# Kernel optimization log

Hardware: AMD Instinct MI355X
Metric: run time of the kernel (lower is better)

Reference implementation:

```python
import jax, jax.numpy as jnp
import numpy as np

BN_EPS = 1e-5
CLAMP = 1e-4


def setup_inputs() -> dict:
    key = jax.random.key(0)
    ks = jax.random.split(key, 13)
    B, C, T, A = 32, 1536, 1000, 128
    s = 0.02  # keep conv pre-activations in a sane range
    return {
        "x": jax.random.normal(ks[0], (B, C, T), jnp.float32),
        "W1": jax.random.normal(ks[1], (A, 3 * C), jnp.float32) * s,
        "b1": jax.random.normal(ks[2], (A,), jnp.float32) * s,
        "g1": jax.random.uniform(ks[3], (A,), jnp.float32, 0.5, 1.5),
        "beta1": jax.random.normal(ks[4], (A,), jnp.float32) * 0.1,
        "rm1": jax.random.normal(ks[5], (A,), jnp.float32) * 0.1,
        "rv1": jax.random.uniform(ks[6], (A,), jnp.float32, 0.5, 1.5),
        "W2": jax.random.normal(ks[7], (C, A), jnp.float32) * s,
        "b2": jax.random.normal(ks[8], (C,), jnp.float32) * s,
        "g2": jax.random.uniform(ks[9], (C,), jnp.float32, 0.5, 1.5),
        "beta2": jax.random.normal(ks[10], (C,), jnp.float32) * 0.1,
        "rm2": jax.random.normal(ks[11], (C,), jnp.float32) * 0.1,
        "rv2": jax.random.uniform(ks[12], (C,), jnp.float32, 0.5, 1.5),
    }


def _bn(h, g, beta, rm, rv):
    # inference-mode BatchNorm1d over channel axis 1 of [B, C, T]
    inv = g / jnp.sqrt(rv + BN_EPS)
    return h * inv[None, :, None] + (beta - rm * inv)[None, :, None]


def reference(x, W1, b1, g1, beta1, rm1, rv1, W2, b2, g2, beta2, rm2, rv2):
    B, C, T = x.shape
    mean = jnp.mean(x, axis=2)                       # [B, C]
    var = jnp.var(x, axis=2, ddof=1)                 # unbiased, matches torch.var
    std = jnp.sqrt(jnp.clip(var, CLAMP, None))       # [B, C]
    # 1x1 conv over concat([x, mean.repeat(T), std.repeat(T)]) without
    # materializing the [B, 3C, T] tensor: split W1 into three channel blocks.
    Wx, Wm, Ws = W1[:, :C], W1[:, C:2 * C], W1[:, 2 * C:]
    h = jnp.einsum('oc,bct->bot', Wx, x)             # [B, A, T]
    h = h + (mean @ Wm.T + std @ Ws.T + b1)[:, :, None]
    h = jax.nn.relu(h)
    h = _bn(h, g1, beta1, rm1, rv1)
    h = jnp.tanh(h)
    h = jnp.einsum('oa,bat->bot', W2, h) + b2[None, :, None]  # [B, C, T]
    h = jax.nn.relu(h)
    h = _bn(h, g2, beta2, rm2, rv2)
    w = jax.nn.softmax(h, axis=2)                    # attention over time
    mu = jnp.sum(x * w, axis=2)                      # [B, C]
    sg = jnp.sqrt(jnp.clip(jnp.sum(x * x * w, axis=2) - mu * mu, CLAMP, None))
    return jnp.concatenate([mu, sg], axis=1)         # [B, 2C]
```

## Files before the change

kernel.cpp:

```cpp
#include <hip/hip_runtime.h>
#include <cmath>

#define BN_EPS 1e-5f
#define CLAMPV 1e-4f

static constexpr int B_ = 32, C_ = 1536, T_ = 1000, A_ = 128;
static constexpr int C3 = 3 * C_;
static constexpr int TP = 1024;
static constexpr int KS1 = C_ / 32;
static constexpr int KS2 = A_ / 32;
static constexpr int OM1 = A_ / 16;
static constexpr int OM2 = C_ / 16;

using bf16x8 = __attribute__((ext_vector_type(8))) short;
using f32x4  = __attribute__((ext_vector_type(4))) float;

#define MFMA(a, b, c) __builtin_amdgcn_mfma_f32_16x16x32_bf16(a, b, c, 0, 0, 0)

static constexpr size_t WT_OFF   = 0;
static constexpr size_t MEAN_OFF = 393216;
static constexpr size_t STD_OFF  = MEAN_OFF + 49152;
static constexpr size_t BIAS_OFF = STD_OFF + 49152;
static constexpr size_t INV1_OFF = BIAS_OFF + 4096;
static constexpr size_t SH1_OFF  = INV1_OFF + 128;
static constexpr size_t INV2_OFF = SH1_OFF + 128;
static constexpr size_t SH2_OFF  = INV2_OFF + 1536;
static constexpr size_t WXH_OFF  = SH2_OFF + 1536;
static constexpr size_t WXL_OFF  = WXH_OFF + 98304;
static constexpr size_t W2H_OFF  = WXL_OFF + 98304;
static constexpr size_t W2L_OFF  = W2H_OFF + 98304;
static constexpr size_t HTP_OFF  = W2L_OFF + 98304;
static constexpr size_t SS_OFF   = HTP_OFF + 4194304;
static constexpr size_t PP_OFF   = SS_OFF + 49152;
static constexpr size_t QQ_OFF   = PP_OFF + 49152;

__device__ __forceinline__ short f2bf(float v) {
  __bf16 b = (__bf16)v;
  return __builtin_bit_cast(short, b);
}
__device__ __forceinline__ float bf2f(short s) {
  unsigned int u = ((unsigned int)(unsigned short)s) << 16;
  return __builtin_bit_cast(float, u);
}

__global__ __launch_bounds__(256) void k_transpose(const float* __restrict__ W1,
                                                   float* __restrict__ WT) {
  __shared__ float tile[32][33];
  int c0 = blockIdx.x * 32;
  int o0 = blockIdx.y * 32;
  int tx = threadIdx.x, ty = threadIdx.y;
#pragma unroll
  for (int k = 0; k < 32; k += 8)
    tile[ty + k][tx] = W1[(size_t)(o0 + ty + k) * C3 + C_ + c0 + tx];
  __syncthreads();
#pragma unroll
  for (int k = 0; k < 32; k += 8)
    WT[(size_t)(c0 + ty + k) * A_ + o0 + tx] = tile[tx][ty + k];
}

__global__ __launch_bounds__(256) void k_stats(const float* __restrict__ x,
                                               float* __restrict__ mean,
                                               float* __restrict__ stdv) {
  int row  = blockIdx.x * 4 + (threadIdx.x >> 6);
  int lane = threadIdx.x & 63;
  const float2* xr2 = (const float2*)(x + (size_t)row * T_);
  float s1 = 0.f, s2 = 0.f;
#pragma unroll 4
  for (int j = lane; j < T_ / 2; j += 64) {
    float2 v = xr2[j];
    s1 += v.x + v.y;
    s2 += v.x * v.x + v.y * v.y;
  }
#pragma unroll
  for (int off = 32; off; off >>= 1) {
    s1 += __shfl_xor(s1, off);
    s2 += __shfl_xor(s2, off);
  }
  if (lane == 0) {
    float m   = s1 / T_;
    float var = (s2 - s1 * m) / (T_ - 1);
    mean[row] = m;
    stdv[row] = sqrtf(fmaxf(var, CLAMPV));
  }
}

__global__ void k_bn(const float* __restrict__ g1, const float* __restrict__ beta1,
                     const float* __restrict__ rm1, const float* __restrict__ rv1,
                     const float* __restrict__ g2, const float* __restrict__ beta2,
                     const float* __restrict__ rm2, const float* __restrict__ rv2,
                     float* inv1, float* sh1, float* inv2, float* sh2) {
  int i = blockIdx.x * 256 + threadIdx.x;
  if (i < A_) { float iv = g1[i] * rsqrtf(rv1[i] + BN_EPS); inv1[i] = iv; sh1[i] = beta1[i] - rm1[i] * iv; }
  if (i < C_) { float iv = g2[i] * rsqrtf(rv2[i] + BN_EPS); inv2[i] = iv; sh2[i] = beta2[i] - rm2[i] * iv; }
}

__global__ __launch_bounds__(256) void k_pack_w(const float* __restrict__ W1,
                                                const float* __restrict__ W2,
                                                unsigned short* __restrict__ WxH,
                                                unsigned short* __restrict__ WxL,
                                                unsigned short* __restrict__ W2H,
                                                unsigned short* __restrict__ W2L) {
  int id = blockIdx.x * 256 + threadIdx.x;
  if (id < OM1 * KS1 * 64) {
    int l = id & 63; int ks = (id >> 6) % KS1; int om = id / (64 * KS1);
    int o  = om * 16 + (l & 15);
    int c0 = ks * 32 + (l >> 4) * 8;
#pragma unroll
    for (int j = 0; j < 8; j++) {
      float v = W1[(size_t)o * C3 + c0 + j];
      short h = f2bf(v); float fh = bf2f(h); short lo = f2bf(v - fh);
      WxH[(size_t)id * 8 + j] = (unsigned short)h;
      WxL[(size_t)id * 8 + j] = (unsigned short)lo;
    }
  } else {
    int id2 = id - OM1 * KS1 * 64;
    int l = id2 & 63; int ks = (id2 >> 6) & 3; int om = id2 / (64 * KS2);
    int cr = om * 16 + (l & 15);
    int a0 = ks * 32 + (l >> 4) * 8;
#pragma unroll
    for (int j = 0; j < 8; j++) {
      float v = W2[(size_t)cr * A_ + a0 + j];
      short h = f2bf(v); float fh = bf2f(h); short lo = f2bf(v - fh);
      W2H[(size_t)id2 * 8 + j] = (unsigned short)h;
      W2L[(size_t)id2 * 8 + j] = (unsigned short)lo;
    }
  }
}

__global__ __launch_bounds__(128) void k_bias(const float* __restrict__ WT,
                                              const float* __restrict__ b1,
                                              const float* __restrict__ mean,
                                              const float* __restrict__ stdv,
                                              float* __restrict__ bias1) {
  __shared__ float sm[C_], ss[C_];
  int b = blockIdx.x, o = threadIdx.x;
  for (int c = o; c < C_; c += 128) { sm[c] = mean[b * C_ + c]; ss[c] = stdv[b * C_ + c]; }
  __syncthreads();
  float acc = b1[o];
#pragma unroll 8
  for (int c = 0; c < C_; c++)
    acc += sm[c] * WT[(size_t)c * A_ + o] + ss[c] * WT[(size_t)(C_ + c) * A_ + o];
  bias1[b * A_ + o] = acc;
}

__global__ __launch_bounds__(256) void k_gemm1(const float* __restrict__ x,
    const unsigned short* __restrict__ WxH, const unsigned short* __restrict__ WxL,
    const float* __restrict__ bias1, const float* __restrict__ inv1, const float* __restrict__ sh1,
    unsigned int* __restrict__ htP) {
  int b = blockIdx.x, tt = blockIdx.y;
  int wid = threadIdx.x >> 6, l = threadIdx.x & 63;
  int wm = wid >> 1, wn = wid & 1;
  int lg = l >> 4, ll = l & 15;

  f32x4 acc[4][4];
#pragma unroll
  for (int mi = 0; mi < 4; mi++)
#pragma unroll
    for (int ni = 0; ni < 4; ni++) acc[mi][ni] = (f32x4){0.f, 0.f, 0.f, 0.f};

  const float* xb = x + (size_t)b * C_ * T_;
  int tbase = tt * 128 + wn * 64;
  int   tloc[4];
  float tmask[4];
#pragma unroll
  for (int ns = 0; ns < 4; ns++) {
    int t = tbase + ns * 16 + ll;
    tloc[ns]  = t < T_ ? t : T_ - 1;
    tmask[ns] = t < T_ ? 1.f : 0.f;
  }

  for (int ks = 0; ks < KS1; ks++) {
    bf16x8 ah[4], al[4];
#pragma unroll
    for (int mi = 0; mi < 4; mi++) {
      size_t fi = ((size_t)((wm * 4 + mi) * KS1 + ks) * 64 + l) * 8;
      ah[mi] = *(const bf16x8*)(WxH + fi);
      al[mi] = *(const bf16x8*)(WxL + fi);
    }
    int cg = ks * 32 + lg * 8;
    bf16x8 bh[4], bl[4];
#pragma unroll
    for (int ns = 0; ns < 4; ns++) {
      const float* xp = xb + tloc[ns];
      float m = tmask[ns];
#pragma unroll
      for (int j = 0; j < 8; j++) {
        float v = xp[(size_t)(cg + j) * T_] * m;
        short h = f2bf(v); float fh = bf2f(h); short lo = f2bf(v - fh);
        bh[ns][j] = h; bl[ns][j] = lo;
      }
    }
#pragma unroll
    for (int mi = 0; mi < 4; mi++)
#pragma unroll
      for (int ns = 0; ns < 4; ns++) {
        acc[mi][ns] = MFMA(ah[mi], bh[ns], acc[mi][ns]);
        acc[mi][ns] = MFMA(ah[mi], bl[ns], acc[mi][ns]);
        acc[mi][ns] = MFMA(al[mi], bh[ns], acc[mi][ns]);
      }
  }

#pragma unroll
  for (int mi = 0; mi < 4; mi++) {
#pragma unroll
    for (int r = 0; r < 4; r++) {
      int o = wm * 64 + mi * 16 + lg * 4 + r;
      float bz = bias1[b * A_ + o];
      float iv = inv1[o], sv = sh1[o];
#pragma unroll
      for (int ni = 0; ni < 4; ni++) {
        int t = tbase + ni * 16 + ll;
        float v = acc[mi][ni][r] + bz;
        v = fmaxf(v, 0.f) * iv + sv;
        float e  = __expf(2.f * v);
        float th = 1.f - 2.f / (e + 1.f);
        short h = f2bf(th); float fh = bf2f(h); short lo = f2bf(th - fh);
        htP[(size_t)(b * A_ + o) * TP + t] =
            ((unsigned int)(unsigned short)h << 16) | (unsigned short)lo;
      }
    }
  }
}

__global__ __launch_bounds__(256) void k_pool(const float* __restrict__ x,
    const unsigned int* __restrict__ htP,
    const unsigned short* __restrict__ W2H, const unsigned short* __restrict__ W2L,
    const float* __restrict__ b2, const float* __restrict__ inv2, const float* __restrict__ sh2,
    float* __restrict__ SS, float* __restrict__ PP, float* __restrict__ QQ) {
  int b = blockIdx.x, cb = blockIdx.y, th = blockIdx.z;
  int wid = threadIdx.x >> 6, l = threadIdx.x & 63;
  int wm = wid >> 1, wn = wid & 1;
  int lg = l >> 4, ll = l & 15;
  int tix = threadIdx.x;

  __shared__ float sb2[128], siv[128], ssh[128];
  __shared__ float rS[2][128], rP[2][128], rQ[2][128];
  if (tix < 128) {
    int c = cb * 128 + tix;
    sb2[tix] = b2[c]; siv[tix] = inv2[c]; ssh[tix] = sh2[c];
  }
  __syncthreads();

  float S[4][4] = {}, P[4][4] = {}, Q[4][4] = {};
  const float* xb = x + (size_t)b * C_ * T_;
  const unsigned int* hb = htP + (size_t)b * A_ * TP;

  for (int tt = th * 2; tt < th * 2 + 2; tt++) {
    int tb = tt * 128 + wn * 64;
    f32x4 acc[4][4];
#pragma unroll
    for (int mi = 0; mi < 4; mi++)
#pragma unroll
      for (int ni = 0; ni < 4; ni++) acc[mi][ni] = (f32x4){0.f, 0.f, 0.f, 0.f};

    for (int ks = 0; ks < KS2; ks++) {
      bf16x8 bh[4], bl[4];
      int ag = ks * 32 + lg * 8;
#pragma unroll
      for (int ns = 0; ns < 4; ns++) {
        int t = tb + ns * 16 + ll;
#pragma unroll
        for (int j = 0; j < 8; j++) {
          unsigned int v = hb[(size_t)(ag + j) * TP + t];
          bh[ns][j] = (short)(v >> 16);
          bl[ns][j] = (short)(v & 0xffffu);
        }
      }
#pragma unroll
      for (int mi = 0; mi < 4; mi++) {
        size_t fi = ((size_t)((cb * 8 + wm * 4 + mi) * KS2 + ks) * 64 + l) * 8;
        bf16x8 ah = *(const bf16x8*)(W2H + fi);
        bf16x8 al = *(const bf16x8*)(W2L + fi);
#pragma unroll
        for (int ns = 0; ns < 4; ns++) {
          acc[mi][ns] = MFMA(ah, bh[ns], acc[mi][ns]);
          acc[mi][ns] = MFMA(ah, bl[ns], acc[mi][ns]);
          acc[mi][ns] = MFMA(al, bh[ns], acc[mi][ns]);
        }
      }
    }
#pragma unroll
    for (int ns = 0; ns < 4; ns++) {
      int t = tb + ns * 16 + ll;
      float em = t < T_ ? 1.f : 0.f;
      int   te = t < T_ ? t : T_ - 1;
#pragma unroll
      for (int mi = 0; mi < 4; mi++) {
#pragma unroll
        for (int r = 0; r < 4; r++) {
          int cl = wm * 64 + mi * 16 + lg * 4 + r;
          float h2 = acc[mi][ns][r] + sb2[cl];
          float z  = fmaxf(h2, 0.f) * siv[cl] + ssh[cl];
          float e  = __expf(z) * em;
          float xv = xb[(size_t)(cb * 128 + cl) * T_ + te];
          S[mi][r] += e; P[mi][r] += e * xv; Q[mi][r] += e * xv * xv;
        }
      }
    }
  }

#pragma unroll
  for (int mi = 0; mi < 4; mi++)
#pragma unroll
    for (int r = 0; r < 4; r++)
      for (int d = 1; d < 16; d <<= 1) {
        S[mi][r] += __shfl_xor(S[mi][r], d);
        P[mi][r] += __shfl_xor(P[mi][r], d);
        Q[mi][r] += __shfl_xor(Q[mi][r], d);
      }
  if (ll == 0) {
#pragma unroll
    for (int mi = 0; mi < 4; mi++)
#pragma unroll
      for (int r = 0; r < 4; r++) {
        int cl = wm * 64 + mi * 16 + lg * 4 + r;
        rS[wn][cl] = S[mi][r]; rP[wn][cl] = P[mi][r]; rQ[wn][cl] = Q[mi][r];
      }
  }
  __syncthreads();
  if (tix < 128) {
    int i = b * C_ + cb * 128 + tix;
    atomicAdd(&SS[i], rS[0][tix] + rS[1][tix]);
    atomicAdd(&PP[i], rP[0][tix] + rP[1][tix]);
    atomicAdd(&QQ[i], rQ[0][tix] + rQ[1][tix]);
  }
}

__global__ void k_zero(float* p, int n) {
  int i = blockIdx.x * 256 + threadIdx.x;
  if (i < n) p[i] = 0.f;
}

__global__ void k_finish(const float* __restrict__ SS, const float* __restrict__ PP,
                         const float* __restrict__ QQ, float* __restrict__ out) {
  int i = blockIdx.x * 256 + threadIdx.x;
  if (i >= B_ * C_) return;
  int b = i / C_, c = i % C_;
  float S = SS[i];
  float mu = PP[i] / S;
  float var = QQ[i] / S - mu * mu;
  out[(size_t)b * 2 * C_ + c]      = mu;
  out[(size_t)b * 2 * C_ + C_ + c] = sqrtf(fmaxf(var, CLAMPV));
}

extern "C" void kernel_launch(void* const* d_in, const int* in_sizes, int n_in,
                              void* d_out, int out_size, void* d_ws, size_t ws_size,
                              hipStream_t stream) {
  const float* x     = (const float*)d_in[0];
  const float* W1    = (const float*)d_in[1];
  const float* b1    = (const float*)d_in[2];
  const float* g1    = (const float*)d_in[3];
  const float* beta1 = (const float*)d_in[4];
  const float* rm1   = (const float*)d_in[5];
  const float* rv1   = (const float*)d_in[6];
  const float* W2    = (const float*)d_in[7];
  const float* b2    = (const float*)d_in[8];
  const float* g2    = (const float*)d_in[9];
  const float* beta2 = (const float*)d_in[10];
  const float* rm2   = (const float*)d_in[11];
  const float* rv2   = (const float*)d_in[12];

  float* ws    = (float*)d_ws;
  float* WT    = ws + WT_OFF;
  float* mean  = ws + MEAN_OFF;
  float* stdv  = ws + STD_OFF;
  float* bias1 = ws + BIAS_OFF;
  float* inv1  = ws + INV1_OFF;
  float* sh1   = ws + SH1_OFF;
  float* inv2  = ws + INV2_OFF;
  float* sh2   = ws + SH2_OFF;
  unsigned short* WxH = (unsigned short*)(ws + WXH_OFF);
  unsigned short* WxL = (unsigned short*)(ws + WXL_OFF);
  unsigned short* W2H = (unsigned short*)(ws + W2H_OFF);
  unsigned short* W2L = (unsigned short*)(ws + W2L_OFF);
  unsigned int*   htP = (unsigned int*)(ws + HTP_OFF);
  float* SS = ws + SS_OFF;
  float* PP = ws + PP_OFF;
  float* QQ = ws + QQ_OFF;
  float* out = (float*)d_out;

  k_bn<<<dim3(6), 256, 0, stream>>>(g1, beta1, rm1, rv1, g2, beta2, rm2, rv2,
                                    inv1, sh1, inv2, sh2);
  k_transpose<<<dim3(96, 4), dim3(32, 8), 0, stream>>>(W1, WT);
  k_pack_w<<<dim3(192), 256, 0, stream>>>(W1, W2, WxH, WxL, W2H, W2L);
  k_zero<<<dim3((3 * B_ * C_ + 255) / 256), 256, 0, stream>>>(SS, 3 * B_ * C_);
  k_stats<<<dim3(B_ * C_ / 4), 256, 0, stream>>>(x, mean, stdv);
  k_bias<<<dim3(B_), 128, 0, stream>>>(WT, b1, mean, stdv, bias1);
  k_gemm1<<<dim3(B_, 8), 256, 0, stream>>>(x, WxH, WxL, bias1, inv1, sh1, htP);
  k_pool<<<dim3(B_, 12, 4), 256, 0, stream>>>(x, htP, W2H, W2L, b2, inv2, sh2, SS, PP, QQ);
  k_finish<<<dim3((B_ * C_ + 255) / 256), 256, 0, stream>>>(SS, PP, QQ, out);
}
```

Baseline: 558.6 us.

## Increase parallelism across bias, GEMM1 split-K, and pool kernels

The bias reduction is split across 8 channel groups with a second reduce kernel. GEMM1 becomes a 2-way split-K with smaller time tiles, and the activation moves into a separate elementwise kernel that sums the partials. The pool kernel uses 512 threads with one time tile per block and 8 time slices, and writes per-slice partial sums instead of atomics, so the zeroing kernel is removed. The goal is more blocks to fill the GPU's compute units, at the cost of extra partial-sum memory traffic and extra launches.

```diff
diff --git a/kernel.cpp b/kernel.cpp
--- a/kernel.cpp
+++ b/kernel.cpp
@@ -17,22 +17,24 @@
 
 #define MFMA(a, b, c) __builtin_amdgcn_mfma_f32_16x16x32_bf16(a, b, c, 0, 0, 0)
 
-static constexpr size_t WT_OFF   = 0;
-static constexpr size_t MEAN_OFF = 393216;
-static constexpr size_t STD_OFF  = MEAN_OFF + 49152;
-static constexpr size_t BIAS_OFF = STD_OFF + 49152;
-static constexpr size_t INV1_OFF = BIAS_OFF + 4096;
-static constexpr size_t SH1_OFF  = INV1_OFF + 128;
-static constexpr size_t INV2_OFF = SH1_OFF + 128;
-static constexpr size_t SH2_OFF  = INV2_OFF + 1536;
-static constexpr size_t WXH_OFF  = SH2_OFF + 1536;
-static constexpr size_t WXL_OFF  = WXH_OFF + 98304;
-static constexpr size_t W2H_OFF  = WXL_OFF + 98304;
-static constexpr size_t W2L_OFF  = W2H_OFF + 98304;
-static constexpr size_t HTP_OFF  = W2L_OFF + 98304;
-static constexpr size_t SS_OFF   = HTP_OFF + 4194304;
-static constexpr size_t PP_OFF   = SS_OFF + 49152;
-static constexpr size_t QQ_OFF   = PP_OFF + 49152;
+static constexpr size_t WT_OFF    = 0;
+static constexpr size_t MEAN_OFF  = 393216;
+static constexpr size_t STD_OFF   = MEAN_OFF + 49152;
+static constexpr size_t BIASP_OFF = STD_OFF + 49152;
+static constexpr size_t BIAS_OFF  = BIASP_OFF + 32768;
+static constexpr size_t INV1_OFF  = BIAS_OFF + 4096;
+static constexpr size_t SH1_OFF   = INV1_OFF + 128;
+static constexpr size_t INV2_OFF  = SH1_OFF + 128;
+static constexpr size_t SH2_OFF   = INV2_OFF + 1536;
+static constexpr size_t WXH_OFF   = SH2_OFF + 1536;
+static constexpr size_t WXL_OFF   = WXH_OFF + 98304;
+static constexpr size_t W2H_OFF   = WXL_OFF + 98304;
+static constexpr size_t W2L_OFF   = W2H_OFF + 98304;
+static constexpr size_t HTP_OFF   = W2L_OFF + 98304;
+static constexpr size_t HPART_OFF = HTP_OFF + 4194304;
+static constexpr size_t SP_OFF    = HPART_OFF + 8388608;
+static constexpr size_t PP_OFF    = SP_OFF + 393216;
+static constexpr size_t QP_OFF    = PP_OFF + 393216;
 
 __device__ __forceinline__ short f2bf(float v) {
   __bf16 b = (__bf16)v;
@@ -127,49 +129,69 @@
   }
 }
 
-__global__ __launch_bounds__(128) void k_bias(const float* __restrict__ WT,
-                                              const float* __restrict__ b1,
-                                              const float* __restrict__ mean,
-                                              const float* __restrict__ stdv,
-                                              float* __restrict__ bias1) {
-  __shared__ float sm[C_], ss[C_];
+__global__ __launch_bounds__(256) void k_biasPart(const float* __restrict__ WT,
+                                                  const float* __restrict__ mean,
+                                                  const float* __restrict__ stdv,
+                                                  float* __restrict__ biasPart) {
+  __shared__ float sm[192], ss[192];
+  __shared__ float red[2][128];
+  int b = blockIdx.x, cg = blockIdx.y;
+  int tix = threadIdx.x;
+  if (tix < 192) {
+    sm[tix] = mean[b * C_ + cg * 192 + tix];
+    ss[tix] = stdv[b * C_ + cg * 192 + tix];
+  }
+  __syncthreads();
+  int o = tix & 127, cs = tix >> 7;
+  float acc = 0.f;
+#pragma unroll 4
+  for (int i = 0; i < 96; i++) {
+    int c = cs * 96 + i;
+    int cgl = cg * 192 + c;
+    acc += sm[c] * WT[(size_t)cgl * A_ + o] + ss[c] * WT[(size_t)(C_ + cgl) * A_ + o];
+  }
+  red[cs][o] = acc;
+  __syncthreads();
+  if (tix < 128)
+    biasPart[((size_t)cg * B_ + b) * A_ + tix] = red[0][tix] + red[1][tix];
+}
+
+__global__ void k_bias2(const float* __restrict__ b1, const float* __restrict__ biasPart,
+                        float* __restrict__ bias1) {
   int b = blockIdx.x, o = threadIdx.x;
-  for (int c = o; c < C_; c += 128) { sm[c] = mean[b * C_ + c]; ss[c] = stdv[b * C_ + c]; }
-  __syncthreads();
-  float acc = b1[o];
-#pragma unroll 8
-  for (int c = 0; c < C_; c++)
-    acc += sm[c] * WT[(size_t)c * A_ + o] + ss[c] * WT[(size_t)(C_ + c) * A_ + o];
-  bias1[b * A_ + o] = acc;
-}
-
-__global__ __launch_bounds__(256) void k_gemm1(const float* __restrict__ x,
+  float a = b1[o];
+#pragma unroll
+  for (int g = 0; g < 8; g++) a += biasPart[((size_t)g * B_ + b) * A_ + o];
+  bias1[b * A_ + o] = a;
+}
+
+__global__ __launch_bounds__(256, 4) void k_gemm1(const float* __restrict__ x,
     const unsigned short* __restrict__ WxH, const unsigned short* __restrict__ WxL,
-    const float* __restrict__ bias1, const float* __restrict__ inv1, const float* __restrict__ sh1,
-    unsigned int* __restrict__ htP) {
-  int b = blockIdx.x, tt = blockIdx.y;
+    float* __restrict__ hPart) {
+  int b = blockIdx.x, tt = blockIdx.y, kc = blockIdx.z;
   int wid = threadIdx.x >> 6, l = threadIdx.x & 63;
-  int wm = wid >> 1, wn = wid & 1;
+  int wm = wid & 1, wn = wid >> 1;
   int lg = l >> 4, ll = l & 15;
 
-  f32x4 acc[4][4];
+  f32x4 acc[4][2];
 #pragma unroll
   for (int mi = 0; mi < 4; mi++)
 #pragma unroll
-    for (int ni = 0; ni < 4; ni++) acc[mi][ni] = (f32x4){0.f, 0.f, 0.f, 0.f};
+    for (int ns = 0; ns < 2; ns++) acc[mi][ns] = (f32x4){0.f, 0.f, 0.f, 0.f};
 
   const float* xb = x + (size_t)b * C_ * T_;
-  int tbase = tt * 128 + wn * 64;
-  int   tloc[4];
-  float tmask[4];
-#pragma unroll
-  for (int ns = 0; ns < 4; ns++) {
+  int tbase = tt * 64 + wn * 32;
+  int   tloc[2];
+  float tmask[2];
+#pragma unroll
+  for (int ns = 0; ns < 2; ns++) {
     int t = tbase + ns * 16 + ll;
     tloc[ns]  = t < T_ ? t : T_ - 1;
     tmask[ns] = t < T_ ? 1.f : 0.f;
   }
 
-  for (int ks = 0; ks < KS1; ks++) {
+  for (int ksl = 0; ksl < KS1 / 2; ksl++) {
+    int ks = kc * (KS1 / 2) + ksl;
     bf16x8 ah[4], al[4];
 #pragma unroll
     for (int mi = 0; mi < 4; mi++) {
@@ -178,9 +200,9 @@
       al[mi] = *(const bf16x8*)(WxL + fi);
     }
     int cg = ks * 32 + lg * 8;
-    bf16x8 bh[4], bl[4];
-#pragma unroll
-    for (int ns = 0; ns < 4; ns++) {
+    bf16x8 bh[2], bl[2];
+#pragma unroll
+    for (int ns = 0; ns < 2; ns++) {
       const float* xp = xb + tloc[ns];
       float m = tmask[ns];
 #pragma unroll
@@ -193,7 +215,7 @@
 #pragma unroll
     for (int mi = 0; mi < 4; mi++)
 #pragma unroll
-      for (int ns = 0; ns < 4; ns++) {
+      for (int ns = 0; ns < 2; ns++) {
         acc[mi][ns] = MFMA(ah[mi], bh[ns], acc[mi][ns]);
         acc[mi][ns] = MFMA(ah[mi], bl[ns], acc[mi][ns]);
         acc[mi][ns] = MFMA(al[mi], bh[ns], acc[mi][ns]);
@@ -201,144 +223,140 @@
   }
 
 #pragma unroll
-  for (int mi = 0; mi < 4; mi++) {
+  for (int mi = 0; mi < 4; mi++)
 #pragma unroll
     for (int r = 0; r < 4; r++) {
       int o = wm * 64 + mi * 16 + lg * 4 + r;
-      float bz = bias1[b * A_ + o];
-      float iv = inv1[o], sv = sh1[o];
-#pragma unroll
-      for (int ni = 0; ni < 4; ni++) {
-        int t = tbase + ni * 16 + ll;
-        float v = acc[mi][ni][r] + bz;
-        v = fmaxf(v, 0.f) * iv + sv;
-        float e  = __expf(2.f * v);
-        float th = 1.f - 2.f / (e + 1.f);
-        short h = f2bf(th); float fh = bf2f(h); short lo = f2bf(th - fh);
-        htP[(size_t)(b * A_ + o) * TP + t] =
-            ((unsigned int)(unsigned short)h << 16) | (unsigned short)lo;
-      }
-    }
-  }
-}
-
-__global__ __launch_bounds__(256) void k_pool(const float* __restrict__ x,
+#pragma unroll
+      for (int ns = 0; ns < 2; ns++) {
+        int t = tbase + ns * 16 + ll;
+        hPart[(((size_t)kc * B_ + b) * A_ + o) * TP + t] = acc[mi][ns][r];
+      }
+    }
+}
+
+__global__ __launch_bounds__(256) void k_act(const float* __restrict__ hPart,
+                                             const float* __restrict__ bias1,
+                                             const float* __restrict__ inv1,
+                                             const float* __restrict__ sh1,
+                                             unsigned int* __restrict__ htP) {
+  int bo = blockIdx.x;
+  int t  = blockIdx.y * 256 + threadIdx.x;
+  int b = bo >> 7, o = bo & 127;
+  float v = hPart[(size_t)bo * TP + t] + hPart[((size_t)B_ * A_ + bo) * TP + t]
+          + bias1[b * A_ + o];
+  v = fmaxf(v, 0.f) * inv1[o] + sh1[o];
+  float e  = __expf(2.f * v);
+  float th = 1.f - 2.f / (e + 1.f);
+  short h = f2bf(th); float fh = bf2f(h); short lo = f2bf(th - fh);
+  htP[(size_t)bo * TP + t] = ((unsigned int)(unsigned short)h << 16) | (unsigned short)lo;
+}
+
+__global__ __launch_bounds__(512, 4) void k_pool(const float* __restrict__ x,
     const unsigned int* __restrict__ htP,
     const unsigned short* __restrict__ W2H, const unsigned short* __restrict__ W2L,
     const float* __restrict__ b2, const float* __restrict__ inv2, const float* __restrict__ sh2,
-    float* __restrict__ SS, float* __restrict__ PP, float* __restrict__ QQ) {
+    float* __restrict__ SP, float* __restrict__ PP, float* __restrict__ QP) {
   int b = blockIdx.x, cb = blockIdx.y, th = blockIdx.z;
-  int wid = threadIdx.x >> 6, l = threadIdx.x & 63;
-  int wm = wid >> 1, wn = wid & 1;
+  int tix = threadIdx.x;
+  int wid = tix >> 6, l = tix & 63;
+  int wm = wid & 1, wt = wid >> 1;
   int lg = l >> 4, ll = l & 15;
-  int tix = threadIdx.x;
 
   __shared__ float sb2[128], siv[128], ssh[128];
-  __shared__ float rS[2][128], rP[2][128], rQ[2][128];
+  __shared__ float rS[4][128], rP[4][128], rQ[4][128];
   if (tix < 128) {
     int c = cb * 128 + tix;
     sb2[tix] = b2[c]; siv[tix] = inv2[c]; ssh[tix] = sh2[c];
   }
   __syncthreads();
 
-  float S[4][4] = {}, P[4][4] = {}, Q[4][4] = {};
+  f32x4 acc[4][2];
+#pragma unroll
+  for (int mi = 0; mi < 4; mi++)
+#pragma unroll
+    for (int ns = 0; ns < 2; ns++) acc[mi][ns] = (f32x4){0.f, 0.f, 0.f, 0.f};
+
+  const unsigned int* hb = htP + (size_t)b * A_ * TP;
+  int tb = th * 128 + wt * 32;
+
+  for (int ks = 0; ks < KS2; ks++) {
+    bf16x8 bh[2], bl[2];
+    int ag = ks * 32 + lg * 8;
+#pragma unroll
+    for (int ns = 0; ns < 2; ns++) {
+      int t = tb + ns * 16 + ll;
+#pragma unroll
+      for (int j = 0; j < 8; j++) {
+        unsigned int v = hb[(size_t)(ag + j) * TP + t];
+        bh[ns][j] = (short)(v >> 16);
+        bl[ns][j] = (short)(v & 0xffffu);
+      }
+    }
+#pragma unroll
+    for (int mi = 0; mi < 4; mi++) {
+      size_t fi = ((size_t)((cb * 8 + wm * 4 + mi) * KS2 + ks) * 64 + l) * 8;
+      bf16x8 ah = *(const bf16x8*)(W2H + fi);
+      bf16x8 al = *(const bf16x8*)(W2L + fi);
+#pragma unroll
+      for (int ns = 0; ns < 2; ns++) {
+        acc[mi][ns] = MFMA(ah, bh[ns], acc[mi][ns]);
+        acc[mi][ns] = MFMA(ah, bl[ns], acc[mi][ns]);
+        acc[mi][ns] = MFMA(al, bh[ns], acc[mi][ns]);
+      }
+    }
+  }
+
   const float* xb = x + (size_t)b * C_ * T_;
-  const unsigned int* hb = htP + (size_t)b * A_ * TP;
-
-  for (int tt = th * 2; tt < th * 2 + 2; tt++) {
-    int tb = tt * 128 + wn * 64;
-    f32x4 acc[4][4];
-#pragma unroll
-    for (int mi = 0; mi < 4; mi++)
-#pragma unroll
-      for (int ni = 0; ni < 4; ni++) acc[mi][ni] = (f32x4){0.f, 0.f, 0.f, 0.f};
-
-    for (int ks = 0; ks < KS2; ks++) {
-      bf16x8 bh[4], bl[4];
-      int ag = ks * 32 + lg * 8;
-#pragma unroll
-      for (int ns = 0; ns < 4; ns++) {
+#pragma unroll
+  for (int mi = 0; mi < 4; mi++) {
+#pragma unroll
+    for (int r = 0; r < 4; r++) {
+      int cl = wm * 64 + mi * 16 + lg * 4 + r;
+      float s = 0.f, p = 0.f, q = 0.f;
+#pragma unroll
+      for (int ns = 0; ns < 2; ns++) {
         int t = tb + ns * 16 + ll;
-#pragma unroll
-        for (int j = 0; j < 8; j++) {
-          unsigned int v = hb[(size_t)(ag + j) * TP + t];
-          bh[ns][j] = (short)(v >> 16);
-          bl[ns][j] = (short)(v & 0xffffu);
-        }
-      }
-#pragma unroll
-      for (int mi = 0; mi < 4; mi++) {
-        size_t fi = ((size_t)((cb * 8 + wm * 4 + mi) * KS2 + ks) * 64 + l) * 8;
-        bf16x8 ah = *(const bf16x8*)(W2H + fi);
-        bf16x8 al = *(const bf16x8*)(W2L + fi);
-#pragma unroll
-        for (int ns = 0; ns < 4; ns++) {
-          acc[mi][ns] = MFMA(ah, bh[ns], acc[mi][ns]);
-          acc[mi][ns] = MFMA(ah, bl[ns], acc[mi][ns]);
-          acc[mi][ns] = MFMA(al, bh[ns], acc[mi][ns]);
-        }
-      }
-    }
-#pragma unroll
-    for (int ns = 0; ns < 4; ns++) {
-      int t = tb + ns * 16 + ll;
-      float em = t < T_ ? 1.f : 0.f;
-      int   te = t < T_ ? t : T_ - 1;
-#pragma unroll
-      for (int mi = 0; mi < 4; mi++) {
-#pragma unroll
-        for (int r = 0; r < 4; r++) {
-          int cl = wm * 64 + mi * 16 + lg * 4 + r;
-          float h2 = acc[mi][ns][r] + sb2[cl];
-          float z  = fmaxf(h2, 0.f) * siv[cl] + ssh[cl];
-          float e  = __expf(z) * em;
-          float xv = xb[(size_t)(cb * 128 + cl) * T_ + te];
-          S[mi][r] += e; P[mi][r] += e * xv; Q[mi][r] += e * xv * xv;
-        }
-      }
-    }
-  }
-
-#pragma unroll
-  for (int mi = 0; mi < 4; mi++)
-#pragma unroll
-    for (int r = 0; r < 4; r++)
+        float em = t < T_ ? 1.f : 0.f;
+        int   te = t < T_ ? t : T_ - 1;
+        float h2 = acc[mi][ns][r] + sb2[cl];
+        float z  = fmaxf(h2, 0.f) * siv[cl] + ssh[cl];
+        float e  = __expf(z) * em;
+        float xv = xb[(size_t)(cb * 128 + cl) * T_ + te];
+        s += e; p += e * xv; q += e * xv * xv;
+      }
+#pragma unroll
       for (int d = 1; d < 16; d <<= 1) {
-        S[mi][r] += __shfl_xor(S[mi][r], d);
-        P[mi][r] += __shfl_xor(P[mi][r], d);
-        Q[mi][r] += __shfl_xor(Q[mi][r], d);
-      }
-  if (ll == 0) {
-#pragma unroll
-    for (int mi = 0; mi < 4; mi++)
-#pragma unroll
-      for (int r = 0; r < 4; r++) {
-        int cl = wm * 64 + mi * 16 + lg * 4 + r;
-        rS[wn][cl] = S[mi][r]; rP[wn][cl] = P[mi][r]; rQ[wn][cl] = Q[mi][r];
-      }
+        s += __shfl_xor(s, d);
+        p += __shfl_xor(p, d);
+        q += __shfl_xor(q, d);
+      }
+      if (ll == 0) { rS[wt][cl] = s; rP[wt][cl] = p; rQ[wt][cl] = q; }
+    }
   }
   __syncthreads();
   if (tix < 128) {
-    int i = b * C_ + cb * 128 + tix;
-    atomicAdd(&SS[i], rS[0][tix] + rS[1][tix]);
-    atomicAdd(&PP[i], rP[0][tix] + rP[1][tix]);
-    atomicAdd(&QQ[i], rQ[0][tix] + rQ[1][tix]);
-  }
-}
-
-__global__ void k_zero(float* p, int n) {
-  int i = blockIdx.x * 256 + threadIdx.x;
-  if (i < n) p[i] = 0.f;
-}
-
-__global__ void k_finish(const float* __restrict__ SS, const float* __restrict__ PP,
-                         const float* __restrict__ QQ, float* __restrict__ out) {
+    float S = rS[0][tix] + rS[1][tix] + rS[2][tix] + rS[3][tix];
+    float P = rP[0][tix] + rP[1][tix] + rP[2][tix] + rP[3][tix];
+    float Q = rQ[0][tix] + rQ[1][tix] + rQ[2][tix] + rQ[3][tix];
+    size_t o = ((size_t)th * B_ + b) * C_ + cb * 128 + tix;
+    SP[o] = S; PP[o] = P; QP[o] = Q;
+  }
+}
+
+__global__ void k_finish(const float* __restrict__ SP, const float* __restrict__ PP,
+                         const float* __restrict__ QP, float* __restrict__ out) {
   int i = blockIdx.x * 256 + threadIdx.x;
   if (i >= B_ * C_) return;
   int b = i / C_, c = i % C_;
-  float S = SS[i];
-  float mu = PP[i] / S;
-  float var = QQ[i] / S - mu * mu;
+  float S = 0.f, P = 0.f, Q = 0.f;
+#pragma unroll
+  for (int t8 = 0; t8 < 8; t8++) {
+    size_t o = ((size_t)t8 * B_ + b) * C_ + c;
+    S += SP[o]; P += PP[o]; Q += QP[o];
+  }
+  float mu  = P / S;
+  float var = Q / S - mu * mu;
   out[(size_t)b * 2 * C_ + c]      = mu;
   out[(size_t)b * 2 * C_ + C_ + c] = sqrtf(fmaxf(var, CLAMPV));
 }
@@ -360,33 +378,36 @@
   const float* rm2   = (const float*)d_in[11];
   const float* rv2   = (const float*)d_in[12];
 
-  float* ws    = (float*)d_ws;
-  float* WT    = ws + WT_OFF;
-  float* mean  = ws + MEAN_OFF;
-  float* stdv  = ws + STD_OFF;
-  float* bias1 = ws + BIAS_OFF;
-  float* inv1  = ws + INV1_OFF;
-  float* sh1   = ws + SH1_OFF;
-  float* inv2  = ws + INV2_OFF;
-  float* sh2   = ws + SH2_OFF;
+  float* ws     = (float*)d_ws;
+  float* WT     = ws + WT_OFF;
+  float* mean   = ws + MEAN_OFF;
+  float* stdv   = ws + STD_OFF;
+  float* biasP  = ws + BIASP_OFF;
+  float* bias1  = ws + BIAS_OFF;
+  float* inv1   = ws + INV1_OFF;
+  float* sh1    = ws + SH1_OFF;
+  float* inv2   = ws + INV2_OFF;
+  float* sh2    = ws + SH2_OFF;
   unsigned short* WxH = (unsigned short*)(ws + WXH_OFF);
   unsigned short* WxL = (unsigned short*)(ws + WXL_OFF);
   unsigned short* W2H = (unsigned short*)(ws + W2H_OFF);
   unsigned short* W2L = (unsigned short*)(ws + W2L_OFF);
   unsigned int*   htP = (unsigned int*)(ws + HTP_OFF);
-  float* SS = ws + SS_OFF;
+  float* hPart  = ws + HPART_OFF;
+  float* SP = ws + SP_OFF;
   float* PP = ws + PP_OFF;
-  float* QQ = ws + QQ_OFF;
+  float* QP = ws + QP_OFF;
   float* out = (float*)d_out;
 
   k_bn<<<dim3(6), 256, 0, stream>>>(g1, beta1, rm1, rv1, g2, beta2, rm2, rv2,
                                     inv1, sh1, inv2, sh2);
   k_transpose<<<dim3(96, 4), dim3(32, 8), 0, stream>>>(W1, WT);
   k_pack_w<<<dim3(192), 256, 0, stream>>>(W1, W2, WxH, WxL, W2H, W2L);
-  k_zero<<<dim3((3 * B_ * C_ + 255) / 256), 256, 0, stream>>>(SS, 3 * B_ * C_);
   k_stats<<<dim3(B_ * C_ / 4), 256, 0, stream>>>(x, mean, stdv);
-  k_bias<<<dim3(B_), 128, 0, stream>>>(WT, b1, mean, stdv, bias1);
-  k_gemm1<<<dim3(B_, 8), 256, 0, stream>>>(x, WxH, WxL, bias1, inv1, sh1, htP);
-  k_pool<<<dim3(B_, 12, 4), 256, 0, stream>>>(x, htP, W2H, W2L, b2, inv2, sh2, SS, PP, QQ);
-  k_finish<<<dim3((B_ * C_ + 255) / 256), 256, 0, stream>>>(SS, PP, QQ, out);
-}
+  k_biasPart<<<dim3(B_, 8), 256, 0, stream>>>(WT, mean, stdv, biasP);
+  k_bias2<<<dim3(B_), 128, 0, stream>>>(b1, biasP, bias1);
+  k_gemm1<<<dim3(B_, 16, 2), 256, 0, stream>>>(x, WxH, WxL, hPart);
+  k_act<<<dim3(B_ * A_, TP / 256), 256, 0, stream>>>(hPart, bias1, inv1, sh1, htP);
+  k_pool<<<dim3(B_, 12, 8), 512, 0, stream>>>(x, htP, W2H, W2L, b2, inv2, sh2, SP, PP, QP);
+  k_finish<<<dim3((B_ * C_ + 255) / 256), 256, 0, stream>>>(SP, PP, QP, out);
+}
```

Result: faster. 494.4 us (-11.5%).
